# Optimization experiments

Measured on AMD Instinct MI355X. Metric: run time of the kernel, lower is better.

The kernel has to match this reference:

```python
import jax, jax.numpy as jnp
import numpy as np

NUM_HEADS = 12


def setup_inputs() -> dict:
    key = jax.random.key(0)
    k1, k2, k3 = jax.random.split(key, 3)
    B, N, C = 2, 2048, 768
    x = jax.random.normal(k1, (B, N, C), dtype=jnp.float32)
    # xavier_uniform-ish scaled weights
    w_qkv = jax.random.normal(k2, (C, 3 * C), dtype=jnp.float32) * (1.0 / np.sqrt(C))
    w_proj = jax.random.normal(k3, (C, C), dtype=jnp.float32) * (1.0 / np.sqrt(C))
    b_proj = jnp.zeros((C,), dtype=jnp.float32)
    return {"x": x, "w_qkv": w_qkv, "w_proj": w_proj, "b_proj": b_proj}


def reference(x, w_qkv, w_proj, b_proj):
    B, N, C = x.shape
    H = NUM_HEADS
    D = C // H
    scale = D ** -0.5
    # [B, N, 3, H, D]
    qkv = (x @ w_qkv).reshape(B, N, 3, H, D)
    q = qkv[:, :, 0].transpose(0, 2, 1, 3)  # [B, H, N, D]
    k = qkv[:, :, 1].transpose(0, 2, 1, 3)
    v = qkv[:, :, 2].transpose(0, 2, 1, 3)
    attn = jnp.einsum("bhnd,bhmd->bhnm", q, k) * scale  # [B, H, N, N]
    attn = jax.nn.softmax(attn, axis=-1)  # attn_drop = 0.0 -> identity
    out = jnp.einsum("bhnm,bhmd->bhnd", attn, v)  # [B, H, N, D]
    out = out.transpose(0, 2, 1, 3).reshape(B, N, C)
    return out @ w_proj + b_proj  # proj_drop = 0.0 -> identity
```

## Files before the change

### kernel.cpp

```cpp
#include <hip/hip_runtime.h>
#include <hip/hip_bf16.h>

typedef __attribute__((ext_vector_type(8))) short short8;
typedef __attribute__((ext_vector_type(4))) float f32x4;
typedef __attribute__((ext_vector_type(4))) int int4v;

#define HD 64
#define NH 12
#define SEQ 2048
#define CDIM 768
#define NT (SEQ / 64)

#define QSCALE 0.180336880f

static __device__ __forceinline__ unsigned short f2bf(float f) {
    __hip_bfloat16 h = __float2bfloat16(f);
    return __builtin_bit_cast(unsigned short, h);
}

static __device__ __forceinline__ unsigned cvtpk_bf16(float a, float b) {
    unsigned r;
    asm("v_cvt_pk_bf16_f32 %0, %1, %2" : "=v"(r) : "v"(a), "v"(b));
    return r;
}

#define GLDS16(gp, lp) __builtin_amdgcn_global_load_lds( \
    (const __attribute__((address_space(1))) void*)(gp), \
    (__attribute__((address_space(3))) void*)(lp), 16, 0, 0)

static __device__ __forceinline__ int kperm_f(int r) {
    const int kt = r >> 4, gg = (r >> 2) & 3, jj = r & 3;
    return 32 * (kt & 1) + 8 * gg + 4 * (kt >> 1) + jj;
}

static __device__ __forceinline__ void transpose_tile(const float* __restrict__ in,
        unsigned short* __restrict__ out, int K, int C, int bx, int by,
        float (*t)[33], int tid) {
    const int k0 = bx * 32, c0 = by * 32;
    const int r = tid >> 3, c4 = (tid & 7) * 4;
    const float4 v = *reinterpret_cast<const float4*>(in + (size_t)(k0 + r) * C + c0 + c4);
    t[r][c4 + 0] = v.x; t[r][c4 + 1] = v.y; t[r][c4 + 2] = v.z; t[r][c4 + 3] = v.w;
    __syncthreads();
    ushort4 o;
    o.x = f2bf(t[c4 + 0][r]); o.y = f2bf(t[c4 + 1][r]);
    o.z = f2bf(t[c4 + 2][r]); o.w = f2bf(t[c4 + 3][r]);
    *reinterpret_cast<ushort4*>(out + (size_t)(c0 + r) * K + k0 + c4) = o;
}

__global__ __launch_bounds__(256) void prep_kernel(
        const float* __restrict__ x, const float* __restrict__ wq, const float* __restrict__ wp,
        unsigned short* __restrict__ xb, unsigned short* __restrict__ wqt, unsigned short* __restrict__ wpt) {
    __shared__ float t[32][33];
    const int blk = blockIdx.x, tid = threadIdx.x;
    if (blk < 1728) {
        transpose_tile(wq, wqt, 768, 2304, blk % 24, blk / 24, t, tid);
    } else if (blk < 2304) {
        const int b2 = blk - 1728;
        transpose_tile(wp, wpt, 768, 768, b2 % 24, b2 / 24, t, tid);
    } else {
        const int b3 = blk - 2304;
        #pragma unroll
        for (int it = 0; it < 4; it++) {
            const int i = (b3 * 4 + it) * 256 + tid;
            const float4 v = reinterpret_cast<const float4*>(x)[i];
            ushort4 o;
            o.x = f2bf(v.x); o.y = f2bf(v.y); o.z = f2bf(v.z); o.w = f2bf(v.w);
            reinterpret_cast<ushort4*>(xb)[i] = o;
        }
    }
}

template<int EPI, int BM>
__global__ __launch_bounds__(256, 3) void gemm_kernel(
    const unsigned short* __restrict__ A,
    const unsigned short* __restrict__ Bt,
    const int K, const int N,
    unsigned short* __restrict__ Qo, unsigned short* __restrict__ Ko, unsigned short* __restrict__ Vo,
    float* __restrict__ Cout, const float* __restrict__ bias)
{
    constexpr int MF = (BM == 128) ? 4 : 2;
    const int tid = threadIdx.x;
    const int wave = tid >> 6, lane = tid & 63;
    const int g = lane >> 4, li = lane & 15;
    const int wr = wave >> 1, wc = wave & 1;
    const int m0 = blockIdx.x * BM, n0 = blockIdx.y * 128;

    __shared__ short As[3][BM * 32];
    __shared__ short Bs[3][128 * 32];

    f32x4 acc[MF][4];
    #pragma unroll
    for (int i = 0; i < MF; i++)
        #pragma unroll
        for (int j = 0; j < 4; j++)
            acc[i][j] = (f32x4){0.f, 0.f, 0.f, 0.f};

    const int srow = wave * 16 + (lane >> 2);
    const int scol = (lane & 3) * 8;
    const unsigned short* aSrc = A + (size_t)(m0 + srow) * K + scol;
    const unsigned short* bSrc = Bt + (size_t)(n0 + srow) * K + scol;
    const int d0 = wave * 16 * 32, d1 = (wave * 16 + 64) * 32;
    const size_t rowskip = (size_t)64 * K;

    #define GSTAGE(kk, bb) do { \
        GLDS16(aSrc + (kk) * 32,           &As[bb][d0]); \
        if (BM == 128) GLDS16(aSrc + (kk) * 32 + rowskip, &As[bb][d1]); \
        GLDS16(bSrc + (kk) * 32,           &Bs[bb][d0]); \
        GLDS16(bSrc + (kk) * 32 + rowskip, &Bs[bb][d1]); \
    } while (0)

    #define GWAIT_DEEP do { \
        if (BM == 128) asm volatile("s_waitcnt vmcnt(4)\n\ts_barrier" ::: "memory"); \
        else           asm volatile("s_waitcnt vmcnt(3)\n\ts_barrier" ::: "memory"); \
    } while (0)

    const int nk = K >> 5;
    GSTAGE(0, 0);
    GSTAGE(1, 1);
    GWAIT_DEEP;

    int cur = 0;
    for (int kk = 0; kk < nk; ++kk) {
        const int sbuf = (cur == 0) ? 2 : cur - 1;
        const bool stage = (kk + 2 < nk);
        if (stage) GSTAGE(kk + 2, sbuf);
        const short* Ab = As[cur];
        const short* Bb = Bs[cur];
        short8 af[MF], bfr[4];
        #pragma unroll
        for (int mf = 0; mf < MF; mf++)
            af[mf] = *reinterpret_cast<const short8*>(&Ab[(wr * (BM / 2) + mf * 16 + li) * 32 + 8 * g]);
        #pragma unroll
        for (int nf = 0; nf < 4; nf++)
            bfr[nf] = *reinterpret_cast<const short8*>(&Bb[(wc * 64 + nf * 16 + li) * 32 + 8 * g]);
        __builtin_amdgcn_s_setprio(1);
        #pragma unroll
        for (int mf = 0; mf < MF; mf++)
            #pragma unroll
            for (int nf = 0; nf < 4; nf++)
                acc[mf][nf] = __builtin_amdgcn_mfma_f32_16x16x32_bf16(af[mf], bfr[nf], acc[mf][nf], 0, 0, 0);
        __builtin_amdgcn_s_setprio(0);
        if (stage) GWAIT_DEEP;
        else       asm volatile("s_waitcnt vmcnt(0)\n\ts_barrier" ::: "memory");
        cur = (cur == 2) ? 0 : cur + 1;
    }
    #undef GSTAGE
    #undef GWAIT_DEEP

    #pragma unroll
    for (int mf = 0; mf < MF; mf++) {
        #pragma unroll
        for (int nf = 0; nf < 4; nf++) {
            #pragma unroll
            for (int j = 0; j < 4; j++) {
                const int r = m0 + wr * (BM / 2) + mf * 16 + 4 * g + j;
                const int c = n0 + wc * 64 + nf * 16 + li;
                const float v = acc[mf][nf][j];
                if (EPI == 0) {
                    const int s = c / 768, rem = c % 768;
                    const int hh = rem >> 6, d = rem & 63;
                    const int bb = r >> 11, n = r & (SEQ - 1);
                    if (s == 0)
                        Qo[(((size_t)bb * NH + hh) * SEQ + n) * HD + d] = f2bf(v * QSCALE);
                    else if (s == 1)
                        Ko[(((size_t)bb * NH + hh) * SEQ + n) * HD + d] = f2bf(v);
                    else
                        Vo[(((size_t)bb * NH + hh) * HD + d) * SEQ + n] = f2bf(v);
                } else {
                    Cout[(size_t)r * N + c] = v + bias[c];
                }
            }
        }
    }
}


static __device__ __forceinline__ void qk_mfma(
    f32x4 (&s)[4], const short* kb, int sl0, int sl1, int li,
    const short8 qf0, const short8 qf1)
{
    #pragma unroll
    for (int kt = 0; kt < 4; kt++) s[kt] = (f32x4){0.f, 0.f, 0.f, 0.f};
    __builtin_amdgcn_s_setprio(1);
    #pragma unroll
    for (int kt = 0; kt < 4; kt++) {
        const short8 ka0 = *reinterpret_cast<const short8*>(&kb[(16 * kt + li) * 64 + sl0]);
        const short8 ka1 = *reinterpret_cast<const short8*>(&kb[(16 * kt + li) * 64 + sl1]);
        s[kt] = __builtin_amdgcn_mfma_f32_16x16x32_bf16(ka0, qf0, s[kt], 0, 0, 0);
        s[kt] = __builtin_amdgcn_mfma_f32_16x16x32_bf16(ka1, qf1, s[kt], 0, 0, 0);
    }
    __builtin_amdgcn_s_setprio(0);
}

static __device__ __forceinline__ void sm_pv(
    const f32x4 (&s)[4], const short* vb, int sl0, int sl1, int li,
    const short8 ones, f32x4 (&o_acc)[4], f32x4& l_acc)
{
    float p[4][4];
    #pragma unroll
    for (int kt = 0; kt < 4; kt++)
        #pragma unroll
        for (int j = 0; j < 4; j++)
            p[kt][j] = __builtin_amdgcn_exp2f(s[kt][j]);

    const int4v i0 = { (int)cvtpk_bf16(p[0][0], p[0][1]), (int)cvtpk_bf16(p[0][2], p[0][3]),
                       (int)cvtpk_bf16(p[2][0], p[2][1]), (int)cvtpk_bf16(p[2][2], p[2][3]) };
    const int4v i1 = { (int)cvtpk_bf16(p[1][0], p[1][1]), (int)cvtpk_bf16(p[1][2], p[1][3]),
                       (int)cvtpk_bf16(p[3][0], p[3][1]), (int)cvtpk_bf16(p[3][2], p[3][3]) };
    const short8 pa0 = __builtin_bit_cast(short8, i0);
    const short8 pa1 = __builtin_bit_cast(short8, i1);

    __builtin_amdgcn_s_setprio(1);
    l_acc = __builtin_amdgcn_mfma_f32_16x16x32_bf16(ones, pa0, l_acc, 0, 0, 0);
    l_acc = __builtin_amdgcn_mfma_f32_16x16x32_bf16(ones, pa1, l_acc, 0, 0, 0);
    #pragma unroll
    for (int nf = 0; nf < 4; nf++) {
        const short8 va0 = *reinterpret_cast<const short8*>(&vb[(16 * nf + li) * 64 + sl0]);
        const short8 va1 = *reinterpret_cast<const short8*>(&vb[(16 * nf + li) * 64 + sl1]);
        o_acc[nf] = __builtin_amdgcn_mfma_f32_16x16x32_bf16(va0, pa0, o_acc[nf], 0, 0, 0);
        o_acc[nf] = __builtin_amdgcn_mfma_f32_16x16x32_bf16(va1, pa1, o_acc[nf], 0, 0, 0);
    }
    __builtin_amdgcn_s_setprio(0);
}

__global__ __launch_bounds__(256, 3) void attn_kernel(
    const unsigned short* __restrict__ Q,
    const unsigned short* __restrict__ Kg,
    const unsigned short* __restrict__ Vtg,
    unsigned short* __restrict__ O)
{
    const int tid = threadIdx.x;
    const int wave = tid >> 6, lane = tid & 63;
    const int g = lane >> 4, li = lane & 15;
    const int head = blockIdx.y;
    const int b = head / NH, h = head % NH;
    const int q0 = blockIdx.x * 64 + wave * 16;
    const size_t plane = (size_t)head * SEQ * HD;

    __shared__ short Ks[2][64 * 64];
    __shared__ short Vs[3][64 * 64];

    short8 qf0, qf1;
    {
        const unsigned short* qp = Q + plane + (size_t)(q0 + li) * HD + 8 * g;
        qf0 = *reinterpret_cast<const short8*>(qp);
        qf1 = *reinterpret_cast<const short8*>(qp + 32);
    }
    const short8 ones = {0x3F80, 0x3F80, 0x3F80, 0x3F80, 0x3F80, 0x3F80, 0x3F80, 0x3F80};

    const int lr = lane >> 3;
    const int colS = ((lane & 7) ^ lr) * 8;
    const int rA = wave * 16 + lr;
    const int rB = rA + 8;
    const unsigned short* kSrcA = Kg + plane + (size_t)kperm_f(rA) * HD + colS;
    const unsigned short* kSrcB = Kg + plane + (size_t)kperm_f(rB) * HD + colS;
    const unsigned short* vSrcA = Vtg + plane + (size_t)rA * SEQ + colS;
    const unsigned short* vSrcB = Vtg + plane + (size_t)rB * SEQ + colS;
    const int stA = wave * 1024, stB = stA + 512;

    #define STAGE(kv, kbuf, vdst) do { \
        GLDS16(kSrcA + (size_t)(kv) * HD, &Ks[kbuf][stA]); \
        GLDS16(kSrcB + (size_t)(kv) * HD, &Ks[kbuf][stB]); \
        GLDS16(vSrcA + (kv),              (vdst) + stA); \
        GLDS16(vSrcB + (kv),              (vdst) + stB); \
    } while (0)

    f32x4 o_acc[4], l_acc;
    #pragma unroll
    for (int nf = 0; nf < 4; nf++) o_acc[nf] = (f32x4){0.f, 0.f, 0.f, 0.f};
    l_acc = (f32x4){0.f, 0.f, 0.f, 0.f};

    const int sl0 = (g ^ (li & 7)) * 8;
    const int sl1 = ((g + 4) ^ (li & 7)) * 8;

    short* vbP = &Vs[2][0];
    short* vbC = &Vs[0][0];
    short* vbN = &Vs[1][0];

    f32x4 sA[4], sB[4];

    STAGE(0, 0, vbC);
    asm volatile("s_waitcnt vmcnt(0)\n\ts_barrier" ::: "memory");

    #define ITER(IT, SC, SP, DOP) do { \
        if ((IT) + 1 < NT) STAGE(((IT) + 1) * 64, ((IT) + 1) & 1, vbN); \
        qk_mfma(SC, &Ks[(IT) & 1][0], sl0, sl1, li, qf0, qf1); \
        if (DOP) sm_pv(SP, vbP, sl0, sl1, li, ones, o_acc, l_acc); \
        asm volatile("s_waitcnt vmcnt(0)\n\ts_barrier" ::: "memory"); \
        { short* t_ = vbP; vbP = vbC; vbC = vbN; vbN = t_; } \
    } while (0)

    for (int pr = 0; pr < NT / 2; ++pr) {
        ITER(pr * 2,     sA, sB, pr > 0);
        ITER(pr * 2 + 1, sB, sA, true);
    }
    #undef ITER
    #undef STAGE

    sm_pv(sB, vbP, sl0, sl1, li, ones, o_acc, l_acc);

    const float inv = 1.0f / l_acc[0];
    unsigned short* dst = O + ((size_t)b * SEQ + q0 + li) * CDIM + h * HD + 4 * g;
    #pragma unroll
    for (int nf = 0; nf < 4; nf++) {
        ushort4 o;
        o.x = f2bf(o_acc[nf][0] * inv);
        o.y = f2bf(o_acc[nf][1] * inv);
        o.z = f2bf(o_acc[nf][2] * inv);
        o.w = f2bf(o_acc[nf][3] * inv);
        *reinterpret_cast<ushort4*>(dst + 16 * nf) = o;
    }
}

extern "C" void kernel_launch(void* const* d_in, const int* in_sizes, int n_in,
                              void* d_out, int out_size, void* d_ws, size_t ws_size,
                              hipStream_t stream) {
    const float* x      = (const float*)d_in[0];
    const float* w_qkv  = (const float*)d_in[1];
    const float* w_proj = (const float*)d_in[2];
    const float* b_proj = (const float*)d_in[3];
    float* out = (float*)d_out;

    char* p = (char*)d_ws;
    auto take = [&](size_t bytes) { char* r = p; p += (bytes + 255) & ~(size_t)255; return r; };
    unsigned short* xb      = (unsigned short*)take((size_t)4096 * 768 * 2);
    unsigned short* wqkv_t  = (unsigned short*)take((size_t)2304 * 768 * 2);
    unsigned short* wproj_t = (unsigned short*)take((size_t)768 * 768 * 2);
    unsigned short* Qb      = (unsigned short*)take((size_t)24 * 2048 * 64 * 2);
    unsigned short* Kb      = (unsigned short*)take((size_t)24 * 2048 * 64 * 2);
    unsigned short* Vb      = (unsigned short*)take((size_t)24 * 2048 * 64 * 2);
    unsigned short* Ob      = (unsigned short*)take((size_t)4096 * 768 * 2);

    prep_kernel<<<3072, 256, 0, stream>>>(x, w_qkv, w_proj, xb, wqkv_t, wqkv_t == nullptr ? nullptr : wproj_t);
    gemm_kernel<0, 128><<<dim3(32, 18), 256, 0, stream>>>(xb, wqkv_t, 768, 2304, Qb, Kb, Vb, nullptr, nullptr);
    attn_kernel<<<dim3(32, 24), 256, 0, stream>>>(Qb, Kb, Vb, Ob);
    gemm_kernel<1, 64><<<dim3(64, 6), 256, 0, stream>>>(Ob, wproj_t, 768, 768, nullptr, nullptr, nullptr, out, b_proj);
}
```

Measured before the change: 94.39 us.

## Load V fragments directly to registers and remap blocks per XCD by head

V tiles are no longer staged through shared memory. Each wave now loads its V MFMA fragments straight from global memory into registers one iteration ahead, which cuts LDS traffic and frees LDS space. The grid is flattened and remapped so that the blocks of each head land on the same XCD, aiming for better L2 reuse of K and V. The cost is more VGPRs for the double-buffered V fragments and less coalesced global loads, since each lane reads 16 bytes from separate rows.

```diff
diff --git a/kernel.cpp b/kernel.cpp
--- a/kernel.cpp
+++ b/kernel.cpp
@@ -192,8 +192,20 @@
     __builtin_amdgcn_s_setprio(0);
 }
 
+static __device__ __forceinline__ void loadv(
+    short8 (&v0)[4], short8 (&v1)[4],
+    const unsigned short* vBase, int li, int g, int kv)
+{
+    #pragma unroll
+    for (int nf = 0; nf < 4; nf++) {
+        const unsigned short* p = vBase + (size_t)(16 * nf + li) * SEQ + 8 * g + kv;
+        v0[nf] = *reinterpret_cast<const short8*>(p);
+        v1[nf] = *reinterpret_cast<const short8*>(p + 32);
+    }
+}
+
 static __device__ __forceinline__ void sm_pv(
-    const f32x4 (&s)[4], const short* vb, int sl0, int sl1, int li,
+    const f32x4 (&s)[4], const short8 (&v0)[4], const short8 (&v1)[4],
     const short8 ones, f32x4 (&o_acc)[4], f32x4& l_acc)
 {
     float p[4][4];
@@ -215,10 +227,8 @@
     l_acc = __builtin_amdgcn_mfma_f32_16x16x32_bf16(ones, pa1, l_acc, 0, 0, 0);
     #pragma unroll
     for (int nf = 0; nf < 4; nf++) {
-        const short8 va0 = *reinterpret_cast<const short8*>(&vb[(16 * nf + li) * 64 + sl0]);
-        const short8 va1 = *reinterpret_cast<const short8*>(&vb[(16 * nf + li) * 64 + sl1]);
-        o_acc[nf] = __builtin_amdgcn_mfma_f32_16x16x32_bf16(va0, pa0, o_acc[nf], 0, 0, 0);
-        o_acc[nf] = __builtin_amdgcn_mfma_f32_16x16x32_bf16(va1, pa1, o_acc[nf], 0, 0, 0);
+        o_acc[nf] = __builtin_amdgcn_mfma_f32_16x16x32_bf16(v0[nf], pa0, o_acc[nf], 0, 0, 0);
+        o_acc[nf] = __builtin_amdgcn_mfma_f32_16x16x32_bf16(v1[nf], pa1, o_acc[nf], 0, 0, 0);
     }
     __builtin_amdgcn_s_setprio(0);
 }
@@ -232,13 +242,16 @@
     const int tid = threadIdx.x;
     const int wave = tid >> 6, lane = tid & 63;
     const int g = lane >> 4, li = lane & 15;
-    const int head = blockIdx.y;
+
+    const int bid = blockIdx.x;
+    const int xcd = bid & 7, pos = bid >> 3;
+    const int head = xcd * 3 + (pos >> 5);
+    const int qb = pos & 31;
     const int b = head / NH, h = head % NH;
-    const int q0 = blockIdx.x * 64 + wave * 16;
+    const int q0 = qb * 64 + wave * 16;
     const size_t plane = (size_t)head * SEQ * HD;
 
     __shared__ short Ks[2][64 * 64];
-    __shared__ short Vs[3][64 * 64];
 
     short8 qf0, qf1;
     {
@@ -254,15 +267,12 @@
     const int rB = rA + 8;
     const unsigned short* kSrcA = Kg + plane + (size_t)kperm_f(rA) * HD + colS;
     const unsigned short* kSrcB = Kg + plane + (size_t)kperm_f(rB) * HD + colS;
-    const unsigned short* vSrcA = Vtg + plane + (size_t)rA * SEQ + colS;
-    const unsigned short* vSrcB = Vtg + plane + (size_t)rB * SEQ + colS;
+    const unsigned short* vBase = Vtg + plane;
     const int stA = wave * 1024, stB = stA + 512;
 
-    #define STAGE(kv, kbuf, vdst) do { \
+    #define STAGEK(kv, kbuf) do { \
         GLDS16(kSrcA + (size_t)(kv) * HD, &Ks[kbuf][stA]); \
         GLDS16(kSrcB + (size_t)(kv) * HD, &Ks[kbuf][stB]); \
-        GLDS16(vSrcA + (kv),              (vdst) + stA); \
-        GLDS16(vSrcB + (kv),              (vdst) + stB); \
     } while (0)
 
     f32x4 o_acc[4], l_acc;
@@ -273,31 +283,28 @@
     const int sl0 = (g ^ (li & 7)) * 8;
     const int sl1 = ((g + 4) ^ (li & 7)) * 8;
 
-    short* vbP = &Vs[2][0];
-    short* vbC = &Vs[0][0];
-    short* vbN = &Vs[1][0];
-
     f32x4 sA[4], sB[4];
-
-    STAGE(0, 0, vbC);
+    short8 vA0[4], vA1[4], vB0[4], vB1[4];
+
+    STAGEK(0, 0);
     asm volatile("s_waitcnt vmcnt(0)\n\ts_barrier" ::: "memory");
 
-    #define ITER(IT, SC, SP, DOP) do { \
-        if ((IT) + 1 < NT) STAGE(((IT) + 1) * 64, ((IT) + 1) & 1, vbN); \
+    #define ITER(IT, SC, SP, VN0, VN1, VC0, VC1, DOP) do { \
+        loadv(VN0, VN1, vBase, li, g, (IT) * 64); \
+        if ((IT) + 1 < NT) STAGEK(((IT) + 1) * 64, ((IT) + 1) & 1); \
         qk_mfma(SC, &Ks[(IT) & 1][0], sl0, sl1, li, qf0, qf1); \
-        if (DOP) sm_pv(SP, vbP, sl0, sl1, li, ones, o_acc, l_acc); \
+        if (DOP) sm_pv(SP, VC0, VC1, ones, o_acc, l_acc); \
         asm volatile("s_waitcnt vmcnt(0)\n\ts_barrier" ::: "memory"); \
-        { short* t_ = vbP; vbP = vbC; vbC = vbN; vbN = t_; } \
     } while (0)
 
     for (int pr = 0; pr < NT / 2; ++pr) {
-        ITER(pr * 2,     sA, sB, pr > 0);
-        ITER(pr * 2 + 1, sB, sA, true);
+        ITER(pr * 2,     sA, sB, vA0, vA1, vB0, vB1, pr > 0);
+        ITER(pr * 2 + 1, sB, sA, vB0, vB1, vA0, vA1, true);
     }
     #undef ITER
-    #undef STAGE
-
-    sm_pv(sB, vbP, sl0, sl1, li, ones, o_acc, l_acc);
+    #undef STAGEK
+
+    sm_pv(sB, vB0, vB1, ones, o_acc, l_acc);
 
     const float inv = 1.0f / l_acc[0];
     unsigned short* dst = O + ((size_t)b * SEQ + q0 + li) * CDIM + h * HD + 4 * g;
@@ -331,8 +338,8 @@
     unsigned short* Vb      = (unsigned short*)take((size_t)24 * 2048 * 64 * 2);
     unsigned short* Ob      = (unsigned short*)take((size_t)4096 * 768 * 2);
 
-    prep_kernel<<<3072, 256, 0, stream>>>(x, w_qkv, w_proj, xb, wqkv_t, wqkv_t == nullptr ? nullptr : wproj_t);
+    prep_kernel<<<3072, 256, 0, stream>>>(x, w_qkv, w_proj, xb, wqkv_t, wproj_t);
     gemm_kernel<0, 128><<<dim3(32, 18), 256, 0, stream>>>(xb, wqkv_t, 768, 2304, Qb, Kb, Vb, nullptr, nullptr);
-    attn_kernel<<<dim3(32, 24), 256, 0, stream>>>(Qb, Kb, Vb, Ob);
+    attn_kernel<<<768, 256, 0, stream>>>(Qb, Kb, Vb, Ob);
     gemm_kernel<1, 64><<<dim3(64, 6), 256, 0, stream>>>(Ob, wproj_t, 768, 768, nullptr, nullptr, nullptr, out, b_proj);
 }
```

Measured after the change: 156.2 us. +65.4%, slower.
